# Kernel optimization log

Measured on AMD Instinct MI355X. Metric: run time of the kernel, lower is better.

## Reference

```python
import jax, jax.numpy as jnp
import numpy as np

N_NODES = 100000


def sage_conv(x, edge_index, W_l, W_r, b):
    # PyG SAGEConv (aggr='mean', root_weight=True):
    # out_i = (mean_{j in N(i)} x_j) @ W_l + x_i @ W_r + b
    src, dst = edge_index[0], edge_index[1]
    msgs = x[src]                                             # [E, F] gather
    summed = jax.ops.segment_sum(msgs, dst, num_segments=N_NODES)
    deg = jax.ops.segment_sum(jnp.ones((edge_index.shape[1],), x.dtype), dst,
                              num_segments=N_NODES)
    mean = summed / jnp.maximum(deg, 1.0)[:, None]            # [N, F]
    return mean @ W_l + x @ W_r + b


def setup_inputs() -> dict:
    key = jax.random.key(0)
    ks = jax.random.split(key, 12)
    F, H = 128, 128
    E = 1600000
    s = lambda k, shp, fan: jax.random.normal(k, shp, jnp.float32) / np.sqrt(fan)
    return {
        "x": jax.random.normal(ks[0], (N_NODES, F), jnp.float32),
        "edge_index": jax.random.randint(ks[1], (2, E), 0, N_NODES, jnp.int64),
        "W1_l": s(ks[2], (F, H), F), "W1_r": s(ks[3], (F, H), F),
        "b1": jnp.zeros((H,), jnp.float32),
        "W2_l": s(ks[4], (H, H), H), "W2_r": s(ks[5], (H, H), H),
        "b2": jnp.zeros((H,), jnp.float32),
        "W3_l": s(ks[6], (H, 1), H), "W3_r": s(ks[7], (H, 1), H),
        "b3": jnp.zeros((1,), jnp.float32),
    }


def reference(x, edge_index, W1_l, W1_r, b1, W2_l, W2_r, b2, W3_l, W3_r, b3):
    h = jax.nn.relu(sage_conv(x, edge_index, W1_l, W1_r, b1))
    h = jax.nn.relu(sage_conv(h, edge_index, W2_l, W2_r, b2))
    h = sage_conv(h, edge_index, W3_l, W3_r, b3)   # [N, 1]
    return h.mean(axis=1)                          # [N]
```

## Files before the change

kernel.cpp:

```cpp
#include <hip/hip_runtime.h>


#define NN 100000
#define NB 391
#define SLAB 5120

typedef short bf16x8 __attribute__((ext_vector_type(8)));
typedef float f32x4 __attribute__((ext_vector_type(4)));

static __device__ __forceinline__ float uaf(unsigned u) { return __uint_as_float(u); }
static __device__ __forceinline__ unsigned short f2bf(float f) {
  unsigned u = __float_as_uint(f);
  u += 0x7fffu + ((u >> 16) & 1u);
  return (unsigned short)(u >> 16);
}

__global__ __launch_bounds__(256) void k_prep(
    const int* __restrict__ src, const int* __restrict__ dst, int E, int SB,
    int* __restrict__ cursor, unsigned* __restrict__ pairs,
    const float* __restrict__ x, unsigned short* __restrict__ Z1,
    unsigned short* __restrict__ Z2,
    const float* __restrict__ W1l, const float* __restrict__ W1r,
    const float* __restrict__ W2l, const float* __restrict__ W2r,
    unsigned short* __restrict__ wt1h, unsigned short* __restrict__ wt1l,
    unsigned short* __restrict__ wt2h, unsigned short* __restrict__ wt2l) {
  __shared__ int h[NB];
  __shared__ int rb[NB];
  const int b = blockIdx.x;
  const int tid = threadIdx.x;
  const int XB = NN * 16 / 256;

  if (b < SB) {
    for (int i = tid; i < NB; i += 256) h[i] = 0;
    __syncthreads();
    int s[8], d[8];
    const int base = b * 2048 + tid * 8;
    #pragma unroll
    for (int i = 0; i < 8; i++) {
      int g = base + i;
      bool ok = g < E;
      s[i] = ok ? src[g] : 0;
      d[i] = ok ? dst[g] : -1;
      if (ok) atomicAdd(&h[d[i] >> 8], 1);
    }
    __syncthreads();
    for (int i = tid; i < NB; i += 256) {
      rb[i] = h[i] ? atomicAdd(&cursor[i], h[i]) : 0;
      h[i] = 0;
    }
    __syncthreads();
    #pragma unroll
    for (int i = 0; i < 8; i++) {
      if (d[i] >= 0) {
        int bk = d[i] >> 8;
        int off = rb[bk] + atomicAdd(&h[bk], 1);
        if (off < SLAB)
          pairs[(size_t)bk * SLAB + off] =
              ((unsigned)(d[i] & 255) << 17) | (unsigned)s[i];
      }
    }
  } else if (b < SB + XB) {
    int t = (b - SB) * 256 + tid;
    int node = t >> 4, c = t & 15;
    const float4* xp = (const float4*)(x + (size_t)node * 128 + c * 8);
    float4 a = xp[0], bb = xp[1];
    float v[8] = {a.x, a.y, a.z, a.w, bb.x, bb.y, bb.z, bb.w};
    unsigned hh[8];
    #pragma unroll
    for (int i = 0; i < 8; i++) hh[i] = f2bf(v[i]);
    uint4 p;
    p.x = hh[0] | (hh[1] << 16); p.y = hh[2] | (hh[3] << 16);
    p.z = hh[4] | (hh[5] << 16); p.w = hh[6] | (hh[7] << 16);
    *(uint4*)(Z1 + (size_t)node * 256 + 128 + c * 8) = p;
  } else if (b < SB + XB + 64) {
    #pragma unroll
    for (int it = 0; it < 4; it++) {
      int t = (b - SB - XB) * 1024 + it * 256 + tid;
      int layer = t >> 15;
      int rem = t & 32767;
      int k = rem >> 7;
      int nn = rem & 127;
      const float* Wl = layer ? W2l : W1l;
      const float* Wr = layer ? W2r : W1r;
      float v = (k < 128) ? Wl[k * 128 + nn] : Wr[(k - 128) * 128 + nn];
      unsigned short hv = f2bf(v);
      unsigned short lv = f2bf(v - uaf(((unsigned)hv) << 16));
      (layer ? wt2h : wt1h)[nn * 256 + k] = hv;
      (layer ? wt2l : wt1l)[nn * 256 + k] = lv;
    }
  } else {
    unsigned* z1r = (unsigned*)(Z1 + (size_t)NN * 256);
    unsigned* z2r = (unsigned*)(Z2 + (size_t)NN * 256);
    if (tid < 128) z1r[tid] = 0;
    else z2r[tid - 128] = 0;
  }
}

__global__ __launch_bounds__(256) void k_build(const unsigned* __restrict__ pairs,
                                               const int* __restrict__ cursor,
                                               int* __restrict__ beg, int* __restrict__ deg,
                                               int* __restrict__ csr, int N) {
  __shared__ int cnt[256];
  __shared__ int sd[256];
  __shared__ int cur[256];
  const int b = blockIdx.x;
  const int tid = threadIdx.x;
  const size_t p0 = (size_t)b * SLAB;
  int count = cursor[b];
  if (count > SLAB) count = SLAB;
  cnt[tid] = 0;
  cur[tid] = 0;
  __syncthreads();
  for (int i = tid; i < count; i += 256) atomicAdd(&cnt[pairs[p0 + i] >> 17], 1);
  __syncthreads();
  int v = cnt[tid];
  sd[tid] = v;
  __syncthreads();
  #pragma unroll
  for (int off = 1; off < 256; off <<= 1) {
    int u = (tid >= off) ? sd[tid - off] : 0;
    __syncthreads();
    sd[tid] += u;
    __syncthreads();
  }
  const int node = b * 256 + tid;
  if (node < N) {
    beg[node] = (int)p0 + (sd[tid] - v);
    deg[node] = v;
  }
  __syncthreads();
  for (int i = tid; i < count; i += 256) {
    unsigned pv = pairs[p0 + i];
    int dl = pv >> 17;
    int pos = (sd[dl] - cnt[dl]) + atomicAdd(&cur[dl], 1);
    csr[p0 + pos] = pv & 0x1ffff;
  }
}

#define ACC8(v)                                   \
  acc[0] += uaf((v).x << 16);                     \
  acc[1] += uaf((v).x & 0xffff0000u);             \
  acc[2] += uaf((v).y << 16);                     \
  acc[3] += uaf((v).y & 0xffff0000u);             \
  acc[4] += uaf((v).z << 16);                     \
  acc[5] += uaf((v).z & 0xffff0000u);             \
  acc[6] += uaf((v).w << 16);                     \
  acc[7] += uaf((v).w & 0xffff0000u);

__global__ __launch_bounds__(256) void k_aggZ(unsigned short* __restrict__ Z,
                                              const int* __restrict__ begA,
                                              const int* __restrict__ degA,
                                              const int* __restrict__ csr, int n) {
  const int wid = (blockIdx.x * blockDim.x + threadIdx.x) >> 6;
  const int lane = threadIdx.x & 63;
  if (wid >= n) return;
  const int beg = begA[wid];
  const int d = degA[wid];
  const int g = lane >> 4, c = lane & 15;
  float acc[8] = {0.f, 0.f, 0.f, 0.f, 0.f, 0.f, 0.f, 0.f};

  for (int base = 0; base < d; base += 64) {
    int m = d - base;
    if (m > 64) m = 64;
    int idx = csr[beg + base + (lane < m ? lane : 0)];
    for (int k = 0; k < m; k += 32) {
      uint4 vA[4], vB[4];
      const bool hasB = (k + 16) < m;
      #pragma unroll
      for (int u = 0; u < 4; u++) {
        int kk = k + u * 4 + g;
        int j = __shfl(idx, kk & 63);
        j = (kk < m) ? j : NN;
        vA[u] = *(const uint4*)(Z + (size_t)j * 256 + 128 + c * 8);
      }
      if (hasB) {
        #pragma unroll
        for (int u = 0; u < 4; u++) {
          int kk = k + 16 + u * 4 + g;
          int j = __shfl(idx, kk & 63);
          j = (kk < m) ? j : NN;
          vB[u] = *(const uint4*)(Z + (size_t)j * 256 + 128 + c * 8);
        }
      }
      #pragma unroll
      for (int u = 0; u < 4; u++) { ACC8(vA[u]); }
      if (hasB) {
        #pragma unroll
        for (int u = 0; u < 4; u++) { ACC8(vB[u]); }
      }
    }
  }
  #pragma unroll
  for (int j = 0; j < 8; j++) {
    acc[j] += __shfl_xor(acc[j], 16);
    acc[j] += __shfl_xor(acc[j], 32);
  }
  const float inv = d > 0 ? 1.0f / (float)d : 0.f;
  if (g == 0) {
    unsigned h[8];
    #pragma unroll
    for (int j = 0; j < 8; j++) h[j] = f2bf(acc[j] * inv);
    uint4 p;
    p.x = h[0] | (h[1] << 16); p.y = h[2] | (h[3] << 16);
    p.z = h[4] | (h[5] << 16); p.w = h[6] | (h[7] << 16);
    *(uint4*)(Z + (size_t)wid * 256 + c * 8) = p;
  }
}

template <int MODE>
__global__ __launch_bounds__(256, 2) void k_sage2(
    const unsigned short* __restrict__ Z, const unsigned short* __restrict__ WTh,
    const unsigned short* __restrict__ WTl, const float* __restrict__ bias,
    unsigned short* __restrict__ outB,
    const float* __restrict__ w3l, const float* __restrict__ w3r,
    float* __restrict__ s2, float* __restrict__ r2, int n) {
  const int tid = threadIdx.x;
  const int lane = tid & 63;
  const int w = tid >> 6;
  const int ln = lane & 15;
  const int r16 = lane >> 4;
  const int m0 = blockIdx.x * 256 + w * 64;

  f32x4 acc[4][8];
  #pragma unroll
  for (int s = 0; s < 4; s++)
    #pragma unroll
    for (int cc = 0; cc < 8; cc++) {
      acc[s][cc][0] = 0.f; acc[s][cc][1] = 0.f;
      acc[s][cc][2] = 0.f; acc[s][cc][3] = 0.f;
    }
  float bv[8];
  #pragma unroll
  for (int cc = 0; cc < 8; cc++) bv[cc] = bias[cc * 16 + ln];

  const size_t wbase = (size_t)ln * 256 + r16 * 8;

  #pragma unroll
  for (int kh = 0; kh < 2; kh++) {
    bf16x8 a[4][4];
    #pragma unroll
    for (int s = 0; s < 4; s++) {
      int row = m0 + s * 16 + ln;
      if (row > n - 1) row = n - 1;
      const unsigned short* zp = Z + (size_t)row * 256 + kh * 128 + r16 * 8;
      #pragma unroll
      for (int ks = 0; ks < 4; ks++) a[s][ks] = *(const bf16x8*)(zp + ks * 32);
    }
    #pragma unroll
    for (int ks = 0; ks < 4; ks++) {
      #pragma unroll
      for (int cg = 0; cg < 4; cg++) {
        bf16x8 bh[2], bl[2];
        #pragma unroll
        for (int j = 0; j < 2; j++) {
          const size_t o = wbase + (size_t)(cg * 2 + j) * 4096 + kh * 128 + ks * 32;
          bh[j] = *(const bf16x8*)(WTh + o);
          bl[j] = *(const bf16x8*)(WTl + o);
        }
        #pragma unroll
        for (int j = 0; j < 2; j++) {
          #pragma unroll
          for (int s = 0; s < 4; s++) {
            acc[s][cg * 2 + j] =
                __builtin_amdgcn_mfma_f32_16x16x32_bf16(a[s][ks], bh[j], acc[s][cg * 2 + j], 0, 0, 0);
            acc[s][cg * 2 + j] =
                __builtin_amdgcn_mfma_f32_16x16x32_bf16(a[s][ks], bl[j], acc[s][cg * 2 + j], 0, 0, 0);
          }
        }
      }
    }
  }

  if (MODE == 0) {
    #pragma unroll
    for (int s = 0; s < 4; s++)
      #pragma unroll
      for (int r = 0; r < 4; r++) {
        int node = m0 + s * 16 + r16 * 4 + r;
        if (node < n) {
          unsigned short* op = outB + (size_t)node * 256 + 128 + ln;
          #pragma unroll
          for (int cc = 0; cc < 8; cc++) {
            float v = fmaxf(acc[s][cc][r] + bv[cc], 0.f);
            op[cc * 16] = f2bf(v);
          }
        }
      }
  } else {
    float wl[8], wr[8];
    #pragma unroll
    for (int cc = 0; cc < 8; cc++) {
      wl[cc] = w3l[cc * 16 + ln];
      wr[cc] = w3r[cc * 16 + ln];
    }
    #pragma unroll
    for (int s = 0; s < 4; s++)
      #pragma unroll
      for (int r = 0; r < 4; r++) {
        float sl = 0.f, sr = 0.f;
        #pragma unroll
        for (int cc = 0; cc < 8; cc++) {
          float v = fmaxf(acc[s][cc][r] + bv[cc], 0.f);
          sl += v * wl[cc];
          sr += v * wr[cc];
        }
        sl += __shfl_xor(sl, 1); sl += __shfl_xor(sl, 2);
        sl += __shfl_xor(sl, 4); sl += __shfl_xor(sl, 8);
        sr += __shfl_xor(sr, 1); sr += __shfl_xor(sr, 2);
        sr += __shfl_xor(sr, 4); sr += __shfl_xor(sr, 8);
        int node = m0 + s * 16 + r16 * 4 + r;
        if (ln == 0 && node < n) {
          s2[node] = sl;
          r2[node] = sr;
        }
      }
  }
}

__global__ __launch_bounds__(256) void k_out3(const float* __restrict__ s2,
                                              const float* __restrict__ r2,
                                              const int* __restrict__ beg,
                                              const int* __restrict__ deg,
                                              const int* __restrict__ csr,
                                              const float* __restrict__ b3,
                                              float* __restrict__ out, int n) {
  int t = blockIdx.x * blockDim.x + threadIdx.x;
  int node = t >> 4;
  int ln = t & 15;
  if (node >= n) return;
  int bg = beg[node], d = deg[node];
  float s = 0.f;
  for (int i = ln; i < d; i += 16) s += s2[csr[bg + i]];
  s += __shfl_xor(s, 1); s += __shfl_xor(s, 2);
  s += __shfl_xor(s, 4); s += __shfl_xor(s, 8);
  if (ln == 0) out[node] = s / (d > 0 ? (float)d : 1.0f) + r2[node] + b3[0];
}

extern "C" void kernel_launch(void* const* d_in, const int* in_sizes, int n_in,
                              void* d_out, int out_size, void* d_ws, size_t ws_size,
                              hipStream_t stream) {
  const float* x   = (const float*)d_in[0];
  const int*   ei  = (const int*)d_in[1];
  const float* W1l = (const float*)d_in[2];
  const float* W1r = (const float*)d_in[3];
  const float* b1  = (const float*)d_in[4];
  const float* W2l = (const float*)d_in[5];
  const float* W2r = (const float*)d_in[6];
  const float* b2  = (const float*)d_in[7];
  const float* W3l = (const float*)d_in[8];
  const float* W3r = (const float*)d_in[9];
  const float* b3  = (const float*)d_in[10];
  float* out = (float*)d_out;

  const int N = NN;
  const int E = in_sizes[1] / 2;
  const int* src = ei;
  const int* dst = ei + E;

  char* ws = (char*)d_ws;
  size_t off = 0;
  auto alloc = [&](size_t bytes) -> char* {
    char* p = ws + off;
    off = (off + bytes + 255) & ~(size_t)255;
    return p;
  };
  int* cursor = (int*)alloc((NB + 1) * 4);
  unsigned* pairs = (unsigned*)alloc((size_t)NB * SLAB * 4);
  int* csr  = (int*)alloc((size_t)NB * SLAB * 4);
  int* beg  = (int*)alloc((size_t)N * 4);
  int* deg  = (int*)alloc((size_t)N * 4);
  float* s2 = (float*)alloc((size_t)N * 4);
  float* r2 = (float*)alloc((size_t)N * 4);
  unsigned short* wt1h = (unsigned short*)alloc(128 * 256 * 2);
  unsigned short* wt1l = (unsigned short*)alloc(128 * 256 * 2);
  unsigned short* wt2h = (unsigned short*)alloc(128 * 256 * 2);
  unsigned short* wt2l = (unsigned short*)alloc(128 * 256 * 2);
  unsigned short* Z1 = (unsigned short*)alloc((size_t)(N + 1) * 256 * 2);
  unsigned short* Z2 = (unsigned short*)alloc((size_t)(N + 1) * 256 * 2);

  hipMemsetAsync(cursor, 0, (NB + 1) * 4, stream);

  const int SB = (E + 2047) / 2048;
  const int XB = N * 16 / 256;
  k_prep<<<SB + XB + 64 + 1, 256, 0, stream>>>(
      src, dst, E, SB, cursor, pairs, x, Z1, Z2,
      W1l, W1r, W2l, W2r, wt1h, wt1l, wt2h, wt2l);
  k_build<<<NB, 256, 0, stream>>>(pairs, cursor, beg, deg, csr, N);

  const int wb = (N * 64 + 255) / 256;
  const int sb = (N + 255) / 256;
  k_aggZ<<<wb, 256, 0, stream>>>(Z1, beg, deg, csr, N);
  k_sage2<0><<<sb, 256, 0, stream>>>(Z1, wt1h, wt1l, b1, Z2,
                                     nullptr, nullptr, nullptr, nullptr, N);
  k_aggZ<<<wb, 256, 0, stream>>>(Z2, beg, deg, csr, N);
  k_sage2<1><<<sb, 256, 0, stream>>>(Z2, wt2h, wt2l, b2, nullptr,
                                     W3l, W3r, s2, r2, N);
  k_out3<<<(N * 16 + 255) / 256, 256, 0, stream>>>(s2, r2, beg, deg, csr, b3, out, N);
}
```

Before: 273.7 us.

## Fuse neighbor mean aggregation into the SAGE GEMM kernel via swizzled LDS

Merges the separate aggregation kernel and the MFMA GEMM kernel into one per-layer kernel. Each block first aggregates the neighbor means for its 256 nodes, two nodes per wave iteration to raise memory-level parallelism. It writes them as bf16 into a 64KB XOR-swizzled shared-memory tile, then runs the GEMM reading the mean half from LDS. This removes a global write/read round-trip of the mean features and one launch per layer. In exchange, each block now needs 64KB LDS, which reduces occupancy. Aggregation parallelism also drops from one wave per node to a serial loop of 32 iterations per wave, so latency hiding of the random gathers may suffer.

Result: slower. 305.4 us (+11.6%).

```diff
diff --git a/kernel.cpp b/kernel.cpp
--- a/kernel.cpp
+++ b/kernel.cpp
@@ -137,183 +137,214 @@
   }
 }
 
-#define ACC8(v)                                   \
-  acc[0] += uaf((v).x << 16);                     \
-  acc[1] += uaf((v).x & 0xffff0000u);             \
-  acc[2] += uaf((v).y << 16);                     \
-  acc[3] += uaf((v).y & 0xffff0000u);             \
-  acc[4] += uaf((v).z << 16);                     \
-  acc[5] += uaf((v).z & 0xffff0000u);             \
-  acc[6] += uaf((v).w << 16);                     \
-  acc[7] += uaf((v).w & 0xffff0000u);
-
-__global__ __launch_bounds__(256) void k_aggZ(unsigned short* __restrict__ Z,
-                                              const int* __restrict__ begA,
-                                              const int* __restrict__ degA,
-                                              const int* __restrict__ csr, int n) {
-  const int wid = (blockIdx.x * blockDim.x + threadIdx.x) >> 6;
-  const int lane = threadIdx.x & 63;
-  if (wid >= n) return;
-  const int beg = begA[wid];
-  const int d = degA[wid];
-  const int g = lane >> 4, c = lane & 15;
-  float acc[8] = {0.f, 0.f, 0.f, 0.f, 0.f, 0.f, 0.f, 0.f};
-
-  for (int base = 0; base < d; base += 64) {
-    int m = d - base;
-    if (m > 64) m = 64;
-    int idx = csr[beg + base + (lane < m ? lane : 0)];
-    for (int k = 0; k < m; k += 32) {
-      uint4 vA[4], vB[4];
-      const bool hasB = (k + 16) < m;
-      #pragma unroll
-      for (int u = 0; u < 4; u++) {
-        int kk = k + u * 4 + g;
-        int j = __shfl(idx, kk & 63);
-        j = (kk < m) ? j : NN;
-        vA[u] = *(const uint4*)(Z + (size_t)j * 256 + 128 + c * 8);
-      }
-      if (hasB) {
-        #pragma unroll
-        for (int u = 0; u < 4; u++) {
-          int kk = k + 16 + u * 4 + g;
-          int j = __shfl(idx, kk & 63);
-          j = (kk < m) ? j : NN;
-          vB[u] = *(const uint4*)(Z + (size_t)j * 256 + 128 + c * 8);
-        }
-      }
-      #pragma unroll
-      for (int u = 0; u < 4; u++) { ACC8(vA[u]); }
-      if (hasB) {
-        #pragma unroll
-        for (int u = 0; u < 4; u++) { ACC8(vB[u]); }
-      }
-    }
-  }
-  #pragma unroll
-  for (int j = 0; j < 8; j++) {
-    acc[j] += __shfl_xor(acc[j], 16);
-    acc[j] += __shfl_xor(acc[j], 32);
-  }
-  const float inv = d > 0 ? 1.0f / (float)d : 0.f;
-  if (g == 0) {
-    unsigned h[8];
-    #pragma unroll
-    for (int j = 0; j < 8; j++) h[j] = f2bf(acc[j] * inv);
-    uint4 p;
-    p.x = h[0] | (h[1] << 16); p.y = h[2] | (h[3] << 16);
-    p.z = h[4] | (h[5] << 16); p.w = h[6] | (h[7] << 16);
-    *(uint4*)(Z + (size_t)wid * 256 + c * 8) = p;
-  }
-}
+#define ACC8(A, v)                                \
+  A[0] += uaf((v).x << 16);                       \
+  A[1] += uaf((v).x & 0xffff0000u);               \
+  A[2] += uaf((v).y << 16);                       \
+  A[3] += uaf((v).y & 0xffff0000u);               \
+  A[4] += uaf((v).z << 16);                       \
+  A[5] += uaf((v).z & 0xffff0000u);               \
+  A[6] += uaf((v).w << 16);                       \
+  A[7] += uaf((v).w & 0xffff0000u);
 
 template <int MODE>
-__global__ __launch_bounds__(256, 2) void k_sage2(
-    const unsigned short* __restrict__ Z, const unsigned short* __restrict__ WTh,
-    const unsigned short* __restrict__ WTl, const float* __restrict__ bias,
-    unsigned short* __restrict__ outB,
+__global__ __launch_bounds__(256, 2) void k_fused(
+    const unsigned short* __restrict__ Z,
+    const int* __restrict__ begA, const int* __restrict__ degA,
+    const int* __restrict__ csr,
+    const unsigned short* __restrict__ WTh, const unsigned short* __restrict__ WTl,
+    const float* __restrict__ bias, unsigned short* __restrict__ outB,
     const float* __restrict__ w3l, const float* __restrict__ w3r,
     float* __restrict__ s2, float* __restrict__ r2, int n) {
+  __shared__ __align__(16) unsigned short smem[256 * 128];
   const int tid = threadIdx.x;
   const int lane = tid & 63;
   const int w = tid >> 6;
-  const int ln = lane & 15;
-  const int r16 = lane >> 4;
-  const int m0 = blockIdx.x * 256 + w * 64;
-
-  f32x4 acc[4][8];
-  #pragma unroll
-  for (int s = 0; s < 4; s++)
-    #pragma unroll
-    for (int cc = 0; cc < 8; cc++) {
-      acc[s][cc][0] = 0.f; acc[s][cc][1] = 0.f;
-      acc[s][cc][2] = 0.f; acc[s][cc][3] = 0.f;
-    }
-  float bv[8];
-  #pragma unroll
-  for (int cc = 0; cc < 8; cc++) bv[cc] = bias[cc * 16 + ln];
-
-  const size_t wbase = (size_t)ln * 256 + r16 * 8;
-
-  #pragma unroll
-  for (int kh = 0; kh < 2; kh++) {
-    bf16x8 a[4][4];
-    #pragma unroll
-    for (int s = 0; s < 4; s++) {
-      int row = m0 + s * 16 + ln;
-      if (row > n - 1) row = n - 1;
-      const unsigned short* zp = Z + (size_t)row * 256 + kh * 128 + r16 * 8;
-      #pragma unroll
-      for (int ks = 0; ks < 4; ks++) a[s][ks] = *(const bf16x8*)(zp + ks * 32);
-    }
-    #pragma unroll
-    for (int ks = 0; ks < 4; ks++) {
-      #pragma unroll
-      for (int cg = 0; cg < 4; cg++) {
-        bf16x8 bh[2], bl[2];
+  const int g = lane >> 4, c = lane & 15;
+  const int blk0 = blockIdx.x * 256;
+
+  for (int ii = 0; ii < 64; ii += 2) {
+    const int nd0 = blk0 + w * 64 + ii;
+    const int nd1 = nd0 + 1;
+    int dg0 = 0, bg0 = 0, dg1 = 0, bg1 = 0;
+    if (nd0 < n) { dg0 = degA[nd0]; bg0 = begA[nd0]; }
+    if (nd1 < n) { dg1 = degA[nd1]; bg1 = begA[nd1]; }
+    float acc0[8] = {0.f, 0.f, 0.f, 0.f, 0.f, 0.f, 0.f, 0.f};
+    float acc1[8] = {0.f, 0.f, 0.f, 0.f, 0.f, 0.f, 0.f, 0.f};
+    const int dmax = dg0 > dg1 ? dg0 : dg1;
+
+    for (int base = 0; base < dmax; base += 64) {
+      int m0v = dg0 - base; if (m0v > 64) m0v = 64;
+      int m1v = dg1 - base; if (m1v > 64) m1v = 64;
+      int i0 = csr[bg0 + base + (lane < m0v ? lane : 0)];
+      int i1 = csr[bg1 + base + (lane < m1v ? lane : 0)];
+      const int mm = m0v > m1v ? m0v : m1v;
+      for (int k = 0; k < mm; k += 32) {
+        uint4 vA0[4], vA1[4], vB0[4], vB1[4];
+        const bool hB0 = (k + 16) < m0v;
+        const bool hB1 = (k + 16) < m1v;
         #pragma unroll
-        for (int j = 0; j < 2; j++) {
-          const size_t o = wbase + (size_t)(cg * 2 + j) * 4096 + kh * 128 + ks * 32;
-          bh[j] = *(const bf16x8*)(WTh + o);
-          bl[j] = *(const bf16x8*)(WTl + o);
+        for (int u = 0; u < 4; u++) {
+          int kk = k + u * 4 + g;
+          int j0 = __shfl(i0, kk & 63); j0 = (kk < m0v) ? j0 : NN;
+          int j1 = __shfl(i1, kk & 63); j1 = (kk < m1v) ? j1 : NN;
+          vA0[u] = *(const uint4*)(Z + (size_t)j0 * 256 + 128 + c * 8);
+          vA1[u] = *(const uint4*)(Z + (size_t)j1 * 256 + 128 + c * 8);
+        }
+        if (hB0 | hB1) {
+          #pragma unroll
+          for (int u = 0; u < 4; u++) {
+            int kk = k + 16 + u * 4 + g;
+            int j0 = __shfl(i0, kk & 63); j0 = (kk < m0v) ? j0 : NN;
+            int j1 = __shfl(i1, kk & 63); j1 = (kk < m1v) ? j1 : NN;
+            vB0[u] = *(const uint4*)(Z + (size_t)j0 * 256 + 128 + c * 8);
+            vB1[u] = *(const uint4*)(Z + (size_t)j1 * 256 + 128 + c * 8);
+          }
         }
         #pragma unroll
-        for (int j = 0; j < 2; j++) {
-          #pragma unroll
-          for (int s = 0; s < 4; s++) {
-            acc[s][cg * 2 + j] =
-                __builtin_amdgcn_mfma_f32_16x16x32_bf16(a[s][ks], bh[j], acc[s][cg * 2 + j], 0, 0, 0);
-            acc[s][cg * 2 + j] =
-                __builtin_amdgcn_mfma_f32_16x16x32_bf16(a[s][ks], bl[j], acc[s][cg * 2 + j], 0, 0, 0);
-          }
-        }
-      }
-    }
-  }
-
-  if (MODE == 0) {
+        for (int u = 0; u < 4; u++) { ACC8(acc0, vA0[u]); ACC8(acc1, vA1[u]); }
+        if (hB0 | hB1) {
+          #pragma unroll
+          for (int u = 0; u < 4; u++) { ACC8(acc0, vB0[u]); ACC8(acc1, vB1[u]); }
+        }
+      }
+    }
+    #pragma unroll
+    for (int j = 0; j < 8; j++) {
+      acc0[j] += __shfl_xor(acc0[j], 16);
+      acc0[j] += __shfl_xor(acc0[j], 32);
+      acc1[j] += __shfl_xor(acc1[j], 16);
+      acc1[j] += __shfl_xor(acc1[j], 32);
+    }
+    const float inv0 = dg0 > 0 ? 1.0f / (float)dg0 : 0.f;
+    const float inv1 = dg1 > 0 ? 1.0f / (float)dg1 : 0.f;
+    if (g == 0) {
+      unsigned h0[8], h1[8];
+      #pragma unroll
+      for (int j = 0; j < 8; j++) {
+        h0[j] = f2bf(acc0[j] * inv0);
+        h1[j] = f2bf(acc1[j] * inv1);
+      }
+      uint4 p0, p1;
+      p0.x = h0[0] | (h0[1] << 16); p0.y = h0[2] | (h0[3] << 16);
+      p0.z = h0[4] | (h0[5] << 16); p0.w = h0[6] | (h0[7] << 16);
+      p1.x = h1[0] | (h1[1] << 16); p1.y = h1[2] | (h1[3] << 16);
+      p1.z = h1[4] | (h1[5] << 16); p1.w = h1[6] | (h1[7] << 16);
+      const int r0 = w * 64 + ii, r1 = r0 + 1;
+      *(uint4*)((char*)smem + r0 * 256 + ((c * 16) ^ ((r0 & 7) << 4))) = p0;
+      *(uint4*)((char*)smem + r1 * 256 + ((c * 16) ^ ((r1 & 7) << 4))) = p1;
+    }
+  }
+
+  __syncthreads();
+
+  {
+    const int ln = c;
+    const int r16 = g;
+    const int m0 = blk0 + w * 64;
+
+    f32x4 acc[4][8];
     #pragma unroll
     for (int s = 0; s < 4; s++)
       #pragma unroll
-      for (int r = 0; r < 4; r++) {
-        int node = m0 + s * 16 + r16 * 4 + r;
-        if (node < n) {
-          unsigned short* op = outB + (size_t)node * 256 + 128 + ln;
+      for (int cc = 0; cc < 8; cc++) {
+        acc[s][cc][0] = 0.f; acc[s][cc][1] = 0.f;
+        acc[s][cc][2] = 0.f; acc[s][cc][3] = 0.f;
+      }
+    float bv[8];
+    #pragma unroll
+    for (int cc = 0; cc < 8; cc++) bv[cc] = bias[cc * 16 + ln];
+
+    const size_t wbase = (size_t)ln * 256 + r16 * 8;
+
+    #pragma unroll
+    for (int kh = 0; kh < 2; kh++) {
+      bf16x8 a[4][4];
+      #pragma unroll
+      for (int s = 0; s < 4; s++) {
+        if (kh == 0) {
+          const int rl = w * 64 + s * 16 + ln;
+          const char* lp = (const char*)smem + rl * 256;
+          #pragma unroll
+          for (int ks = 0; ks < 4; ks++)
+            a[s][ks] = *(const bf16x8*)(lp + ((ks * 64 + r16 * 16) ^ ((rl & 7) << 4)));
+        } else {
+          int row = m0 + s * 16 + ln;
+          if (row > n - 1) row = n - 1;
+          const unsigned short* zp = Z + (size_t)row * 256 + 128 + r16 * 8;
+          #pragma unroll
+          for (int ks = 0; ks < 4; ks++) a[s][ks] = *(const bf16x8*)(zp + ks * 32);
+        }
+      }
+      #pragma unroll
+      for (int ks = 0; ks < 4; ks++) {
+        #pragma unroll
+        for (int cg = 0; cg < 4; cg++) {
+          bf16x8 bh[2], bl[2];
+          #pragma unroll
+          for (int j = 0; j < 2; j++) {
+            const size_t o = wbase + (size_t)(cg * 2 + j) * 4096 + kh * 128 + ks * 32;
+            bh[j] = *(const bf16x8*)(WTh + o);
+            bl[j] = *(const bf16x8*)(WTl + o);
+          }
+          #pragma unroll
+          for (int j = 0; j < 2; j++) {
+            #pragma unroll
+            for (int s = 0; s < 4; s++) {
+              acc[s][cg * 2 + j] =
+                  __builtin_amdgcn_mfma_f32_16x16x32_bf16(a[s][ks], bh[j], acc[s][cg * 2 + j], 0, 0, 0);
+              acc[s][cg * 2 + j] =
+                  __builtin_amdgcn_mfma_f32_16x16x32_bf16(a[s][ks], bl[j], acc[s][cg * 2 + j], 0, 0, 0);
+            }
+          }
+        }
+      }
+    }
+
+    if (MODE == 0) {
+      #pragma unroll
+      for (int s = 0; s < 4; s++)
+        #pragma unroll
+        for (int r = 0; r < 4; r++) {
+          int node = m0 + s * 16 + r16 * 4 + r;
+          if (node < n) {
+            unsigned short* op = outB + (size_t)node * 256 + 128 + ln;
+            #pragma unroll
+            for (int cc = 0; cc < 8; cc++) {
+              float v = fmaxf(acc[s][cc][r] + bv[cc], 0.f);
+              op[cc * 16] = f2bf(v);
+            }
+          }
+        }
+    } else {
+      float wl[8], wr[8];
+      #pragma unroll
+      for (int cc = 0; cc < 8; cc++) {
+        wl[cc] = w3l[cc * 16 + ln];
+        wr[cc] = w3r[cc * 16 + ln];
+      }
+      #pragma unroll
+      for (int s = 0; s < 4; s++)
+        #pragma unroll
+        for (int r = 0; r < 4; r++) {
+          float sl = 0.f, sr = 0.f;
           #pragma unroll
           for (int cc = 0; cc < 8; cc++) {
             float v = fmaxf(acc[s][cc][r] + bv[cc], 0.f);
-            op[cc * 16] = f2bf(v);
-          }
-        }
-      }
-  } else {
-    float wl[8], wr[8];
-    #pragma unroll
-    for (int cc = 0; cc < 8; cc++) {
-      wl[cc] = w3l[cc * 16 + ln];
-      wr[cc] = w3r[cc * 16 + ln];
-    }
-    #pragma unroll
-    for (int s = 0; s < 4; s++)
-      #pragma unroll
-      for (int r = 0; r < 4; r++) {
-        float sl = 0.f, sr = 0.f;
-        #pragma unroll
-        for (int cc = 0; cc < 8; cc++) {
-          float v = fmaxf(acc[s][cc][r] + bv[cc], 0.f);
-          sl += v * wl[cc];
-          sr += v * wr[cc];
-        }
-        sl += __shfl_xor(sl, 1); sl += __shfl_xor(sl, 2);
-        sl += __shfl_xor(sl, 4); sl += __shfl_xor(sl, 8);
-        sr += __shfl_xor(sr, 1); sr += __shfl_xor(sr, 2);
-        sr += __shfl_xor(sr, 4); sr += __shfl_xor(sr, 8);
-        int node = m0 + s * 16 + r16 * 4 + r;
-        if (ln == 0 && node < n) {
-          s2[node] = sl;
-          r2[node] = sr;
-        }
-      }
+            sl += v * wl[cc];
+            sr += v * wr[cc];
+          }
+          sl += __shfl_xor(sl, 1); sl += __shfl_xor(sl, 2);
+          sl += __shfl_xor(sl, 4); sl += __shfl_xor(sl, 8);
+          sr += __shfl_xor(sr, 1); sr += __shfl_xor(sr, 2);
+          sr += __shfl_xor(sr, 4); sr += __shfl_xor(sr, 8);
+          int node = m0 + s * 16 + r16 * 4 + r;
+          if (ln == 0 && node < n) {
+            s2[node] = sl;
+            r2[node] = sr;
+          }
+        }
+    }
   }
 }
 
@@ -387,13 +418,10 @@
       W1l, W1r, W2l, W2r, wt1h, wt1l, wt2h, wt2l);
   k_build<<<NB, 256, 0, stream>>>(pairs, cursor, beg, deg, csr, N);
 
-  const int wb = (N * 64 + 255) / 256;
   const int sb = (N + 255) / 256;
-  k_aggZ<<<wb, 256, 0, stream>>>(Z1, beg, deg, csr, N);
-  k_sage2<0><<<sb, 256, 0, stream>>>(Z1, wt1h, wt1l, b1, Z2,
+  k_fused<0><<<sb, 256, 0, stream>>>(Z1, beg, deg, csr, wt1h, wt1l, b1, Z2,
                                      nullptr, nullptr, nullptr, nullptr, N);
-  k_aggZ<<<wb, 256, 0, stream>>>(Z2, beg, deg, csr, N);
-  k_sage2<1><<<sb, 256, 0, stream>>>(Z2, wt2h, wt2l, b2, nullptr,
+  k_fused<1><<<sb, 256, 0, stream>>>(Z2, beg, deg, csr, wt2h, wt2l, b2, nullptr,
                                      W3l, W3r, s2, r2, N);
   k_out3<<<(N * 16 + 255) / 256, 256, 0, stream>>>(s2, r2, beg, deg, csr, b3, out, N);
 }
```
